# Optimization experiments

Hardware: AMD Instinct MI355X
Metric: run time of the kernel (lower is better)

## Reference

```python
import jax, jax.numpy as jnp
import numpy as np

DIM = 2048
NHEAD = 16
HEAD_DIM = DIM // NHEAD
FF_HIDDEN = 5632
EPS = 1e-6


def setup_inputs() -> dict:
    key = jax.random.key(0)
    ks = jax.random.split(key, 8)
    B, S = 2, 2048
    sd = 0.02
    return {
        "x": jax.random.normal(ks[0], (B, S, DIM), dtype=jnp.float32),
        "w_qkv": jax.random.normal(ks[1], (DIM, 3 * DIM), dtype=jnp.float32) * sd,
        "w_out": jax.random.normal(ks[2], (DIM, DIM), dtype=jnp.float32) * sd,
        "g1": jnp.ones((DIM,), dtype=jnp.float32),
        "g2": jnp.ones((DIM,), dtype=jnp.float32),
        "w1": jax.random.normal(ks[3], (DIM, FF_HIDDEN), dtype=jnp.float32) * sd,
        "w3": jax.random.normal(ks[4], (DIM, FF_HIDDEN), dtype=jnp.float32) * sd,
        "w2": jax.random.normal(ks[5], (FF_HIDDEN, DIM), dtype=jnp.float32) * sd,
    }


def _rmsnorm(x, g):
    rms = jnp.sqrt(jnp.mean(x * x, axis=-1, keepdims=True) + EPS)
    return x / rms * g


def _attention(x, w_qkv, w_out):
    B, S, D = x.shape
    qkv = x @ w_qkv  # [B,S,3D]
    q, k, v = jnp.split(qkv, 3, axis=-1)
    # [B,H,S,hd]
    q = q.reshape(B, S, NHEAD, HEAD_DIM).transpose(0, 2, 1, 3)
    k = k.reshape(B, S, NHEAD, HEAD_DIM).transpose(0, 2, 1, 3)
    v = v.reshape(B, S, NHEAD, HEAD_DIM).transpose(0, 2, 1, 3)
    scores = jnp.einsum("bhqd,bhkd->bhqk", q, k) / jnp.sqrt(jnp.float32(HEAD_DIM))
    causal = jnp.tril(jnp.ones((S, S), dtype=bool))
    scores = jnp.where(causal, scores, -jnp.inf)
    attn = jax.nn.softmax(scores, axis=-1)
    out = jnp.einsum("bhqk,bhkd->bhqd", attn, v)
    out = out.transpose(0, 2, 1, 3).reshape(B, S, D)
    return out @ w_out


def _swiglu(x, w1, w3, w2):
    return (jax.nn.silu(x @ w1) * (x @ w3)) @ w2


def reference(x, w_qkv, w_out, g1, g2, w1, w3, w2):
    x = x + _attention(_rmsnorm(x, g1), w_qkv, w_out)
    x = x + _swiglu(_rmsnorm(x, g2), w1, w3, w2)
    return x
```

## Files before the change

### kernel.cpp

```cpp
#include <hip/hip_runtime.h>
#include <hip/hip_bf16.h>
#include <stdint.h>


typedef __attribute__((ext_vector_type(8))) short bf16x8;
typedef __attribute__((ext_vector_type(8))) unsigned short u16x8;
typedef __attribute__((ext_vector_type(4))) float f32x4;

__device__ __forceinline__ unsigned short f2bf(float f) {
  union { float f; unsigned int u; } c; c.f = f;
  unsigned int u = c.u + 0x7fffu + ((c.u >> 16) & 1u);
  return (unsigned short)(u >> 16);
}
__device__ __forceinline__ float bf2f(unsigned short h) {
  union { unsigned int u; float f; } c; c.u = ((unsigned int)h) << 16;
  return c.f;
}

__device__ __forceinline__ void gload16(const void* g, void* l) {
  __builtin_amdgcn_global_load_lds(
      (const __attribute__((address_space(1))) void*)g,
      (__attribute__((address_space(3))) void*)l, 16, 0, 0);
}

__global__ __launch_bounds__(256)
void rmsnorm_bf16(const float* __restrict__ x, const float* __restrict__ g,
                  unsigned short* __restrict__ y)
{
  const long row = blockIdx.x;
  const float* xr = x + row * 2048;
  const int t = threadIdx.x;
  float4 a = *(const float4*)(xr + t * 8);
  float4 b = *(const float4*)(xr + t * 8 + 4);
  float ss = a.x*a.x + a.y*a.y + a.z*a.z + a.w*a.w
           + b.x*b.x + b.y*b.y + b.z*b.z + b.w*b.w;
#pragma unroll
  for (int off = 32; off >= 1; off >>= 1) ss += __shfl_xor(ss, off, 64);
  __shared__ float sm[4];
  if ((t & 63) == 0) sm[t >> 6] = ss;
  __syncthreads();
  float inv = rsqrtf((sm[0] + sm[1] + sm[2] + sm[3]) * (1.0f / 2048.0f) + 1e-6f);
  float4 ga = *(const float4*)(g + t * 8);
  float4 gb = *(const float4*)(g + t * 8 + 4);
  u16x8 ov;
  ov[0] = f2bf(a.x * inv * ga.x); ov[1] = f2bf(a.y * inv * ga.y);
  ov[2] = f2bf(a.z * inv * ga.z); ov[3] = f2bf(a.w * inv * ga.w);
  ov[4] = f2bf(b.x * inv * gb.x); ov[5] = f2bf(b.y * inv * gb.y);
  ov[6] = f2bf(b.z * inv * gb.z); ov[7] = f2bf(b.w * inv * gb.w);
  *(u16x8*)(y + row * 2048 + t * 8) = ov;
}

__global__ __launch_bounds__(256)
void transpose_w(const float* __restrict__ in, unsigned short* __restrict__ outp,
                 int K, int N)
{
  __shared__ float tile[32][33];
  const int c0 = blockIdx.x * 32, r0 = blockIdx.y * 32;
  const int cx = threadIdx.x & 31, ry = threadIdx.x >> 5;
#pragma unroll
  for (int i = 0; i < 4; i++)
    tile[ry + i * 8][cx] = in[(long)(r0 + ry + i * 8) * N + c0 + cx];
  __syncthreads();
#pragma unroll
  for (int i = 0; i < 4; i++)
    outp[(long)(c0 + ry + i * 8) * K + r0 + cx] = f2bf(tile[cx][ry + i * 8]);
}

__global__ __launch_bounds__(256)
void transpose_v(const unsigned short* __restrict__ qkv, unsigned short* __restrict__ vT)
{
  __shared__ unsigned short tile[32][34];
  const int bh = blockIdx.z, b = bh >> 4, hh = bh & 15;
  const int s0 = blockIdx.x * 32, d0 = blockIdx.y * 32;
  const int cx = threadIdx.x & 31, ry = threadIdx.x >> 5;
  const unsigned short* src = qkv + (long)b * 2048 * 6144 + 4096 + hh * 128;
#pragma unroll
  for (int i = 0; i < 4; i++)
    tile[ry + i * 8][cx] = src[(long)(s0 + ry + i * 8) * 6144 + d0 + cx];
  __syncthreads();
  unsigned short* o = vT + ((long)bh * 128 + d0) * 2048 + s0;
#pragma unroll
  for (int i = 0; i < 4; i++)
    o[(long)(ry + i * 8) * 2048 + cx] = tile[cx][ry + i * 8];
}

template<int EPI>
__global__ __launch_bounds__(256)
void gemm_bt(const unsigned short* __restrict__ A,
             const unsigned short* __restrict__ Bt,
             void* __restrict__ Cout,
             const float* __restrict__ res,
             const unsigned short* __restrict__ mulsrc,
             int M, int N, int K)
{
  __shared__ unsigned short lds[2 * 128 * 64];
  const int tid = threadIdx.x;
  const int lane = tid & 63, wave = tid >> 6;
  const int wr = wave >> 1, wc = wave & 1;
  const int l15 = lane & 15, lg = lane >> 4;

  const int nwg = gridDim.x * gridDim.y;
  int wg = blockIdx.y * gridDim.x + blockIdx.x;
  wg = (wg & 7) * (nwg >> 3) + (wg >> 3);
  const int bx = wg % gridDim.x, by = wg / gridDim.x;
  const long m0 = (long)by * 128, n0 = (long)bx * 128;

  f32x4 acc[4][4];
#pragma unroll
  for (int m = 0; m < 4; m++)
#pragma unroll
    for (int n = 0; n < 4; n++) acc[m][n] = f32x4{0.f, 0.f, 0.f, 0.f};

  const int rsub = lane >> 3;
  const int csw  = (lane & 7) ^ rsub;
  const unsigned short* Ab = A  + (m0 + wave * 32 + rsub) * (long)K + csw * 8;
  const unsigned short* Bb = Bt + (n0 + wave * 32 + rsub) * (long)K + csw * 8;
  unsigned short* Al = lds + wave * 2048;
  unsigned short* Bl = lds + 8192 + wave * 2048;

  for (int kt = 0; kt < K; kt += 64) {
    __syncthreads();
#pragma unroll
    for (int i = 0; i < 4; i++) {
      gload16(Ab + (long)(i * 8) * K + kt, Al + i * 512);
      gload16(Bb + (long)(i * 8) * K + kt, Bl + i * 512);
    }
    __syncthreads();
#pragma unroll
    for (int kc = 0; kc < 2; kc++) {
      bf16x8 af[4], bfr[4];
#pragma unroll
      for (int m = 0; m < 4; m++) {
        int row = wr * 64 + m * 16 + l15;
        int off = row * 128 + ((kc * 64 + lg * 16) ^ ((row & 7) << 4));
        af[m] = *(const bf16x8*)((const char*)lds + off);
      }
#pragma unroll
      for (int n = 0; n < 4; n++) {
        int row = wc * 64 + n * 16 + l15;
        int off = 16384 + row * 128 + ((kc * 64 + lg * 16) ^ ((row & 7) << 4));
        bfr[n] = *(const bf16x8*)((const char*)lds + off);
      }
#pragma unroll
      for (int m = 0; m < 4; m++)
#pragma unroll
        for (int n = 0; n < 4; n++)
          acc[m][n] = __builtin_amdgcn_mfma_f32_16x16x32_bf16(af[m], bfr[n], acc[m][n], 0, 0, 0);
    }
  }

  if (EPI == 3) {
#pragma unroll
    for (int m = 0; m < 4; m++)
#pragma unroll
      for (int n = 0; n < 4; n++)
#pragma unroll
        for (int r = 0; r < 4; r++) {
          long row = m0 + wr * 64 + m * 16 + lg * 4 + r;
          long col = n0 + wc * 64 + n * 16 + l15;
          ((float*)Cout)[row * N + col] = acc[m][n][r] + res[row * N + col];
        }
    return;
  }

  __syncthreads();
  unsigned short* Cl = lds;
#pragma unroll
  for (int m = 0; m < 4; m++)
#pragma unroll
    for (int n = 0; n < 4; n++)
#pragma unroll
      for (int r = 0; r < 4; r++) {
        float v = acc[m][n][r];
        if (EPI == 1) v = v / (1.f + __expf(-v));
        Cl[(wr * 64 + m * 16 + lg * 4 + r) * 128 + wc * 64 + n * 16 + l15] = f2bf(v);
      }
  __syncthreads();
#pragma unroll
  for (int r8 = 0; r8 < 8; r8++) {
    int id = tid + r8 * 256;
    int row = id >> 4, c = (id & 15) * 8;
    long grow = m0 + row, gcol = n0 + c;
    u16x8 v = *(const u16x8*)(Cl + row * 128 + c);
    if (EPI == 2) {
      u16x8 mm = *(const u16x8*)(mulsrc + grow * N + gcol);
#pragma unroll
      for (int j = 0; j < 8; j++) v[j] = f2bf(bf2f(v[j]) * bf2f(mm[j]));
    }
    *(u16x8*)((unsigned short*)Cout + grow * N + gcol) = v;
  }
}

#define QSTEP(qf, mrow, lrow, o, qb, isdiag) do {                              \
    f32x4 sacc[4];                                                             \
    __builtin_amdgcn_s_setprio(1);                                             \
    _Pragma("unroll")                                                          \
    for (int cg = 0; cg < 4; cg++) {                                           \
      f32x4 a = f32x4{0.f, 0.f, 0.f, 0.f};                                     \
      _Pragma("unroll")                                                        \
      for (int kc = 0; kc < 4; kc++) {                                         \
        int krow = cg * 16 + l15;                                              \
        bf16x8 kf = *(const bf16x8*)((char*)Klds +                             \
            (krow * 256 + ((kc * 64 + lg * 16) ^ ((krow & 7) << 4))));         \
        a = __builtin_amdgcn_mfma_f32_16x16x32_bf16(qf[kc], kf, a, 0, 0, 0);   \
      }                                                                        \
      sacc[cg] = a;                                                            \
    }                                                                          \
    __builtin_amdgcn_s_setprio(0);                                             \
    float p[4][4], pm[4];                                                      \
    _Pragma("unroll")                                                          \
    for (int r = 0; r < 4; r++) pm[r] = -1e30f;                                \
    _Pragma("unroll")                                                          \
    for (int cg = 0; cg < 4; cg++)                                             \
      _Pragma("unroll")                                                        \
      for (int r = 0; r < 4; r++) {                                            \
        float v = sacc[cg][r] * scale;                                         \
        if (isdiag) {                                                          \
          int kvg = kv0 + cg * 16 + l15;                                       \
          int qg = qb + w * 16 + lg * 4 + r;                                   \
          if (kvg > qg) v = -1e30f;                                            \
        }                                                                      \
        p[cg][r] = v;                                                          \
        pm[r] = fmaxf(pm[r], v);                                               \
      }                                                                        \
    _Pragma("unroll")                                                          \
    for (int r = 0; r < 4; r++) {                                              \
      _Pragma("unroll")                                                        \
      for (int off = 1; off < 16; off <<= 1)                                   \
        pm[r] = fmaxf(pm[r], __shfl_xor(pm[r], off, 64));                      \
      float mn = fmaxf(mrow[r], pm[r]);                                        \
      float al = __expf(mrow[r] - mn);                                         \
      mrow[r] = mn;                                                            \
      float s = 0.f;                                                           \
      _Pragma("unroll")                                                        \
      for (int cg = 0; cg < 4; cg++) { p[cg][r] = __expf(p[cg][r] - mn); s += p[cg][r]; } \
      _Pragma("unroll")                                                        \
      for (int off = 1; off < 16; off <<= 1)                                   \
        s += __shfl_xor(s, off, 64);                                           \
      lrow[r] = lrow[r] * al + s;                                              \
      _Pragma("unroll")                                                        \
      for (int dg = 0; dg < 8; dg++) o[dg][r] *= al;                           \
    }                                                                          \
    _Pragma("unroll")                                                          \
    for (int cg = 0; cg < 4; cg++)                                             \
      _Pragma("unroll")                                                        \
      for (int r = 0; r < 4; r++) {                                            \
        int q = lg * 4 + r;                                                    \
        *((unsigned short*)((char*)&Plds[w][0] +                               \
            (q * 128 + (((cg * 16 + l15) * 2) ^ ((q & 7) << 4))))) = f2bf(p[cg][r]); \
      }                                                                        \
    asm volatile("s_waitcnt lgkmcnt(0)" ::: "memory");                         \
    __builtin_amdgcn_sched_barrier(0);                                         \
    __builtin_amdgcn_s_setprio(1);                                             \
    _Pragma("unroll")                                                          \
    for (int kc = 0; kc < 2; kc++) {                                           \
      bf16x8 pa = *(const bf16x8*)((char*)&Plds[w][0] +                        \
          (l15 * 128 + ((kc * 64 + lg * 16) ^ ((l15 & 7) << 4))));             \
      _Pragma("unroll")                                                        \
      for (int dg = 0; dg < 8; dg++) {                                         \
        int d = dg * 16 + l15;                                                 \
        bf16x8 vf = *(const bf16x8*)((char*)Vlds +                             \
            (d * 128 + ((kc * 64 + lg * 16) ^ ((d & 7) << 4))));               \
        o[dg] = __builtin_amdgcn_mfma_f32_16x16x32_bf16(pa, vf, o[dg], 0, 0, 0); \
      }                                                                        \
    }                                                                          \
    __builtin_amdgcn_s_setprio(0);                                             \
  } while (0)

__global__ __launch_bounds__(256, 2)
void attn_fwd(const unsigned short* __restrict__ qkv,
              const unsigned short* __restrict__ vT,
              unsigned short* __restrict__ out)
{
  __shared__ unsigned short Klds[64 * 128];
  __shared__ unsigned short Vlds[128 * 64];
  __shared__ unsigned short Plds[4][16 * 64];
  const int tid = threadIdx.x, lane = tid & 63, w = tid >> 6;
  const int l15 = lane & 15, lg = lane >> 4;

  const int nwg = gridDim.x * gridDim.y;
  int wg = blockIdx.y * gridDim.x + blockIdx.x;
  wg = (wg & 7) * (nwg >> 3) + (wg >> 3);
  const int ip = wg % 16;
  const int bh = wg / 16;
  const int b = bh >> 4, hh = bh & 15;

  const int qbA = ip * 64, qbB = (31 - ip) * 64;
  const long base = (long)b * 2048 * 6144;
  const int qoff = hh * 128, koff = 2048 + hh * 128;
  const unsigned short* vTg = vT + (long)bh * (128 * 2048);

  bf16x8 qfA[4], qfB[4];
  {
    long qrA = qbA + w * 16 + l15, qrB = qbB + w * 16 + l15;
#pragma unroll
    for (int kc = 0; kc < 4; kc++) {
      qfA[kc] = *(const bf16x8*)(qkv + base + qrA * 6144 + qoff + kc * 32 + lg * 8);
      qfB[kc] = *(const bf16x8*)(qkv + base + qrB * 6144 + qoff + kc * 32 + lg * 8);
    }
  }
  f32x4 oA[8], oB[8];
#pragma unroll
  for (int dg = 0; dg < 8; dg++) {
    oA[dg] = f32x4{0.f, 0.f, 0.f, 0.f};
    oB[dg] = f32x4{0.f, 0.f, 0.f, 0.f};
  }
  float mA[4] = {-1e30f, -1e30f, -1e30f, -1e30f}, lA[4] = {0.f, 0.f, 0.f, 0.f};
  float mB[4] = {-1e30f, -1e30f, -1e30f, -1e30f}, lB[4] = {0.f, 0.f, 0.f, 0.f};
  const float scale = 0.08838834764831845f;

  const int s_st = tid >> 4, d0 = (tid & 15) * 8;
  const int vrow = tid >> 3, vc = tid & 7;

  const int nt = 32 - ip;
  for (int t = 0; t < nt; t++) {
    const int kv0 = t * 64;
#pragma unroll
    for (int u = 0; u < 4; u++) {
      int srow = s_st + u * 16;
      uint4 kk = *(const uint4*)(qkv + base + (long)(kv0 + srow) * 6144 + koff + d0);
      *(uint4*)((char*)Klds + (srow * 256 + ((d0 * 2) ^ ((srow & 7) << 4)))) = kk;
    }
#pragma unroll
    for (int u = 0; u < 4; u++) {
      int d = vrow + u * 32;
      uint4 vv = *(const uint4*)(vTg + (long)d * 2048 + kv0 + vc * 8);
      *(uint4*)((char*)Vlds + (d * 128 + ((vc * 16) ^ ((d & 7) << 4)))) = vv;
    }
    __syncthreads();

    if (t <= ip) QSTEP(qfA, mA, lA, oA, qbA, (t == ip));
    QSTEP(qfB, mB, lB, oB, qbB, (t == nt - 1));

    __syncthreads();
  }

#pragma unroll
  for (int r = 0; r < 4; r++) {
    float invA = 1.f / lA[r], invB = 1.f / lB[r];
    long rowA = (long)b * 2048 + qbA + w * 16 + lg * 4 + r;
    long rowB = (long)b * 2048 + qbB + w * 16 + lg * 4 + r;
#pragma unroll
    for (int dg = 0; dg < 8; dg++) {
      out[rowA * 2048 + hh * 128 + dg * 16 + l15] = f2bf(oA[dg][r] * invA);
      out[rowB * 2048 + hh * 128 + dg * 16 + l15] = f2bf(oB[dg][r] * invB);
    }
  }
}

extern "C" void kernel_launch(void* const* d_in, const int* in_sizes, int n_in,
                              void* d_out, int out_size, void* d_ws, size_t ws_size,
                              hipStream_t stream)
{
  const float* x     = (const float*)d_in[0];
  const float* w_qkv = (const float*)d_in[1];
  const float* w_out = (const float*)d_in[2];
  const float* g1    = (const float*)d_in[3];
  const float* g2    = (const float*)d_in[4];
  const float* w1    = (const float*)d_in[5];
  const float* w3    = (const float*)d_in[6];
  const float* w2    = (const float*)d_in[7];
  float* outp = (float*)d_out;
  char* ws = (char*)d_ws;

  unsigned short* wT  = (unsigned short*)(ws);
  unsigned short* y   = (unsigned short*)(ws + 25165824);
  unsigned short* qkv = (unsigned short*)(ws + 41943040);
  unsigned short* att = (unsigned short*)(ws + 92274688);
  float*          x1  = (float*)(ws + 109051904);
  unsigned short* s1  = (unsigned short*)(ws + 142606336);
  unsigned short* vTb = s1;
  unsigned short* h   = qkv;

  rmsnorm_bf16<<<4096, 256, 0, stream>>>(x, g1, y);
  transpose_w<<<dim3(6144 / 32, 2048 / 32), 256, 0, stream>>>(w_qkv, wT, 2048, 6144);
  gemm_bt<0><<<dim3(48, 32), 256, 0, stream>>>(y, wT, qkv, nullptr, nullptr, 4096, 6144, 2048);
  transpose_v<<<dim3(64, 4, 32), 256, 0, stream>>>(qkv, vTb);
  attn_fwd<<<dim3(16, 32), 256, 0, stream>>>(qkv, vTb, att);
  transpose_w<<<dim3(64, 64), 256, 0, stream>>>(w_out, wT, 2048, 2048);
  gemm_bt<3><<<dim3(16, 32), 256, 0, stream>>>(att, wT, x1, x, nullptr, 4096, 2048, 2048);

  rmsnorm_bf16<<<4096, 256, 0, stream>>>(x1, g2, y);
  transpose_w<<<dim3(176, 64), 256, 0, stream>>>(w1, wT, 2048, 5632);
  gemm_bt<1><<<dim3(44, 32), 256, 0, stream>>>(y, wT, s1, nullptr, nullptr, 4096, 5632, 2048);
  transpose_w<<<dim3(176, 64), 256, 0, stream>>>(w3, wT, 2048, 5632);
  gemm_bt<2><<<dim3(44, 32), 256, 0, stream>>>(y, wT, h, nullptr, s1, 4096, 5632, 2048);
  transpose_w<<<dim3(64, 176), 256, 0, stream>>>(w2, wT, 5632, 2048);
  gemm_bt<3><<<dim3(16, 32), 256, 0, stream>>>(h, wT, outp, x1, nullptr, 4096, 2048, 5632);
}
```

Measured before the change: 716.5 us.

## Add 256x256-tile 8-wave pipelined GEMM for QKV and FFN up projections

Adds a new GEMM kernel that uses 256x256 output tiles with 512 threads, a double-buffered 128KB LDS, swizzled layout, explicit vmcnt/barrier scheduling and raised MFMA priority. It replaces the 128x128 kernel for the QKV, w1 and w3 projections. The aim is more data reuse per LDS load and overlap of global loads with MFMA work. The cost is fewer workgroups (a 384 or 352 block grid), which may leave CUs idle at the tail, plus heavy register and LDS pressure per block.

```diff
diff --git a/kernel.cpp b/kernel.cpp
--- a/kernel.cpp
+++ b/kernel.cpp
@@ -84,6 +84,177 @@
     o[(long)(ry + i * 8) * 2048 + cx] = tile[cx][ry + i * 8];
 }
 
+#define PH_BAR __builtin_amdgcn_s_barrier()
+#define LGKM0 asm volatile("s_waitcnt lgkmcnt(0)" ::: "memory")
+#define VM6 asm volatile("s_waitcnt vmcnt(6)" ::: "memory")
+#define VM0 asm volatile("s_waitcnt vmcnt(0)" ::: "memory")
+
+#define REG_A(buf, kk) ((buf) * 65536 + (kk) * 16384)
+#define REG_B(buf, kk) (32768 + (buf) * 65536 + (kk) * 16384)
+
+#define LDA4(buf, kk, mg) { \
+  a[0] = *(const bf16x8*)(L + REG_A(buf, kk) + aoff + ((mg) + 0) * 1024); \
+  a[1] = *(const bf16x8*)(L + REG_A(buf, kk) + aoff + ((mg) + 1) * 1024); \
+  a[2] = *(const bf16x8*)(L + REG_A(buf, kk) + aoff + ((mg) + 2) * 1024); \
+  a[3] = *(const bf16x8*)(L + REG_A(buf, kk) + aoff + ((mg) + 3) * 1024); }
+
+#define LDB4(buf, kk) { \
+  b[0] = *(const bf16x8*)(L + REG_B(buf, kk) + boff + 0 * 1024); \
+  b[1] = *(const bf16x8*)(L + REG_B(buf, kk) + boff + 1 * 1024); \
+  b[2] = *(const bf16x8*)(L + REG_B(buf, kk) + boff + 2 * 1024); \
+  b[3] = *(const bf16x8*)(L + REG_B(buf, kk) + boff + 3 * 1024); }
+
+#define MM16(mg) { \
+  __builtin_amdgcn_s_setprio(1); \
+  _Pragma("unroll") for (int j = 0; j < 4; j++) \
+    _Pragma("unroll") for (int n = 0; n < 4; n++) \
+      acc[(mg) + j][n] = __builtin_amdgcn_mfma_f32_16x16x32_bf16(a[j], b[n], acc[(mg) + j][n], 0, 0, 0); \
+  __builtin_amdgcn_s_setprio(0); }
+
+#define STGA(buf, kk, tt) { \
+  gload16(As + (long)(tt) * 64 + (kk) * 32,         L + REG_A(buf, kk) + sdst); \
+  gload16(As + rstep + (long)(tt) * 64 + (kk) * 32, L + REG_A(buf, kk) + 8192 + sdst); }
+#define STGB(buf, kk, tt) { \
+  gload16(Bs + (long)(tt) * 64 + (kk) * 32,         L + REG_B(buf, kk) + sdst); \
+  gload16(Bs + rstep + (long)(tt) * 64 + (kk) * 32, L + REG_B(buf, kk) + 8192 + sdst); }
+
+template<int EPI>
+__global__ __launch_bounds__(512, 2)
+void gemm256(const unsigned short* __restrict__ A,
+             const unsigned short* __restrict__ Bt,
+             void* __restrict__ Cout,
+             const float* __restrict__ res,
+             const unsigned short* __restrict__ mulsrc,
+             int M, int N, int K)
+{
+  __shared__ alignas(16) char L[131072];
+  const int tid = threadIdx.x;
+  const int lane = tid & 63, wave = tid >> 6;
+  const int wr = wave >> 2, wc = wave & 3;
+  const int l15 = lane & 15, lg = lane >> 4;
+
+  const int nwg = gridDim.x * gridDim.y;
+  int wg = blockIdx.y * gridDim.x + blockIdx.x;
+  wg = (wg & 7) * (nwg >> 3) + (wg >> 3);
+  const int bx = wg % gridDim.x, by = wg / gridDim.x;
+  const long m0 = (long)by * 256, n0 = (long)bx * 256;
+
+  f32x4 acc[8][4];
+#pragma unroll
+  for (int m = 0; m < 8; m++)
+#pragma unroll
+    for (int n = 0; n < 4; n++) acc[m][n] = f32x4{0.f, 0.f, 0.f, 0.f};
+
+  const int row0 = tid >> 2, cc = tid & 3;
+  const int csw = cc ^ ((row0 >> 1) & 3);
+  const unsigned short* As = A + (m0 + row0) * (long)K + csw * 8;
+  const unsigned short* Bs = Bt + (n0 + row0) * (long)K + csw * 8;
+  const long rstep = (long)128 * K;
+  const int sdst = wave * 1024;
+
+  const int swz = (lg ^ ((l15 >> 1) & 3)) << 4;
+  const int aoff = wr * 8192 + l15 * 64 + swz;
+  const int boff = wc * 4096 + l15 * 64 + swz;
+
+  const int nkt = K >> 6, nit = nkt >> 1;
+
+  STGB(0, 0, 0); STGA(0, 0, 0); STGB(0, 1, 0); STGA(0, 1, 0);
+  STGB(1, 0, 1); STGA(1, 0, 1); STGB(1, 1, 1);
+  VM6;
+  PH_BAR;
+  __builtin_amdgcn_sched_barrier(0);
+
+  for (int it = 0; it < nit; ++it) {
+    const int T = 2 * it;
+    const bool full = (it < nit - 1);
+    bf16x8 a[4], b[4];
+    LDB4(0, 0) LDA4(0, 0, 0)
+    STGA(1, 1, T + 1)
+    PH_BAR; LGKM0;
+    MM16(0)
+    PH_BAR;
+    LDA4(0, 0, 4)
+    if (full) STGB(0, 0, T + 2)
+    PH_BAR; LGKM0;
+    MM16(4)
+    PH_BAR;
+    LDB4(0, 1) LDA4(0, 1, 0)
+    if (full) STGA(0, 0, T + 2)
+    PH_BAR; LGKM0;
+    MM16(0)
+    PH_BAR;
+    LDA4(0, 1, 4)
+    if (full) STGB(0, 1, T + 2)
+    PH_BAR; LGKM0;
+    MM16(4)
+    if (full) { VM6; } else { VM0; }
+    PH_BAR;
+    __builtin_amdgcn_sched_barrier(0);
+    LDB4(1, 0) LDA4(1, 0, 0)
+    if (full) STGA(0, 1, T + 2)
+    PH_BAR; LGKM0;
+    MM16(0)
+    PH_BAR;
+    LDA4(1, 0, 4)
+    if (full) STGB(1, 0, T + 3)
+    PH_BAR; LGKM0;
+    MM16(4)
+    PH_BAR;
+    LDB4(1, 1) LDA4(1, 1, 0)
+    if (full) STGA(1, 0, T + 3)
+    PH_BAR; LGKM0;
+    MM16(0)
+    PH_BAR;
+    LDA4(1, 1, 4)
+    if (full) STGB(1, 1, T + 3)
+    PH_BAR; LGKM0;
+    MM16(4)
+    if (full) { VM6; }
+    PH_BAR;
+    __builtin_amdgcn_sched_barrier(0);
+  }
+
+  if (EPI == 3) {
+#pragma unroll
+    for (int m = 0; m < 8; m++)
+#pragma unroll
+      for (int n = 0; n < 4; n++)
+#pragma unroll
+        for (int r = 0; r < 4; r++) {
+          long row = m0 + wr * 128 + m * 16 + lg * 4 + r;
+          long col = n0 + wc * 64 + n * 16 + l15;
+          ((float*)Cout)[row * N + col] = acc[m][n][r] + res[row * N + col];
+        }
+    return;
+  }
+
+#pragma unroll
+  for (int m = 0; m < 8; m++)
+#pragma unroll
+    for (int n = 0; n < 4; n++)
+#pragma unroll
+      for (int r = 0; r < 4; r++) {
+        float v = acc[m][n][r];
+        if (EPI == 1) v = v / (1.f + __expf(-v));
+        *(unsigned short*)(L + (wr * 128 + m * 16 + lg * 4 + r) * 512
+                             + (wc * 64 + n * 16 + l15) * 2) = f2bf(v);
+      }
+  __syncthreads();
+#pragma unroll
+  for (int rnd = 0; rnd < 16; rnd++) {
+    int id = tid + rnd * 512;
+    int row = id >> 5, c = (id & 31) * 8;
+    u16x8 v = *(const u16x8*)(L + row * 512 + c * 2);
+    long grow = m0 + row, gcol = n0 + c;
+    if (EPI == 2) {
+      u16x8 mm = *(const u16x8*)(mulsrc + grow * N + gcol);
+#pragma unroll
+      for (int j = 0; j < 8; j++) v[j] = f2bf(bf2f(v[j]) * bf2f(mm[j]));
+    }
+    *(u16x8*)((unsigned short*)Cout + grow * N + gcol) = v;
+  }
+}
+
 template<int EPI>
 __global__ __launch_bounds__(256)
 void gemm_bt(const unsigned short* __restrict__ A,
@@ -112,8 +283,8 @@
     for (int n = 0; n < 4; n++) acc[m][n] = f32x4{0.f, 0.f, 0.f, 0.f};
 
   const int rsub = lane >> 3;
-  const int csw  = (lane & 7) ^ rsub;
-  const unsigned short* Ab = A  + (m0 + wave * 32 + rsub) * (long)K + csw * 8;
+  const int csw = (lane & 7) ^ rsub;
+  const unsigned short* Ab = A + (m0 + wave * 32 + rsub) * (long)K + csw * 8;
   const unsigned short* Bb = Bt + (n0 + wave * 32 + rsub) * (long)K + csw * 8;
   unsigned short* Al = lds + wave * 2048;
   unsigned short* Bl = lds + 8192 + wave * 2048;
@@ -373,8 +544,8 @@
   unsigned short* h   = qkv;
 
   rmsnorm_bf16<<<4096, 256, 0, stream>>>(x, g1, y);
-  transpose_w<<<dim3(6144 / 32, 2048 / 32), 256, 0, stream>>>(w_qkv, wT, 2048, 6144);
-  gemm_bt<0><<<dim3(48, 32), 256, 0, stream>>>(y, wT, qkv, nullptr, nullptr, 4096, 6144, 2048);
+  transpose_w<<<dim3(192, 64), 256, 0, stream>>>(w_qkv, wT, 2048, 6144);
+  gemm256<0><<<dim3(24, 16), 512, 0, stream>>>(y, wT, qkv, nullptr, nullptr, 4096, 6144, 2048);
   transpose_v<<<dim3(64, 4, 32), 256, 0, stream>>>(qkv, vTb);
   attn_fwd<<<dim3(16, 32), 256, 0, stream>>>(qkv, vTb, att);
   transpose_w<<<dim3(64, 64), 256, 0, stream>>>(w_out, wT, 2048, 2048);
@@ -382,9 +553,9 @@
 
   rmsnorm_bf16<<<4096, 256, 0, stream>>>(x1, g2, y);
   transpose_w<<<dim3(176, 64), 256, 0, stream>>>(w1, wT, 2048, 5632);
-  gemm_bt<1><<<dim3(44, 32), 256, 0, stream>>>(y, wT, s1, nullptr, nullptr, 4096, 5632, 2048);
+  gemm256<1><<<dim3(22, 16), 512, 0, stream>>>(y, wT, s1, nullptr, nullptr, 4096, 5632, 2048);
   transpose_w<<<dim3(176, 64), 256, 0, stream>>>(w3, wT, 2048, 5632);
-  gemm_bt<2><<<dim3(44, 32), 256, 0, stream>>>(y, wT, h, nullptr, s1, 4096, 5632, 2048);
+  gemm256<2><<<dim3(22, 16), 512, 0, stream>>>(y, wT, h, nullptr, s1, 4096, 5632, 2048);
   transpose_w<<<dim3(64, 176), 256, 0, stream>>>(w2, wT, 5632, 2048);
   gemm_bt<3><<<dim3(16, 32), 256, 0, stream>>>(h, wT, outp, x1, nullptr, 4096, 2048, 5632);
 }
```

Measured after the change: 715.4 us. No clear change (-0.2%).

## Fuse W1/W3 GEMMs into one SwiGLU kernel and double-buffer attention K/V

Applied to the files above, without the earlier changes.

Replaces the two separate FFN up-projection GEMMs, which round-tripped the silu output through memory, with one kernel. It loads the activation tile once and accumulates both W1 and W3 products, then applies silu*mul in the epilogue. Attention now double-buffers K/V tiles in LDS, prefetching the next tile into registers during compute and dropping one barrier per iteration. The trade-off is more registers and LDS per block (two accumulator sets, 48KB LDS), which may lower occupancy.

```diff
diff --git a/kernel.cpp b/kernel.cpp
--- a/kernel.cpp
+++ b/kernel.cpp
@@ -90,7 +90,6 @@
              const unsigned short* __restrict__ Bt,
              void* __restrict__ Cout,
              const float* __restrict__ res,
-             const unsigned short* __restrict__ mulsrc,
              int M, int N, int K)
 {
   __shared__ unsigned short lds[2 * 128 * 64];
@@ -112,8 +111,8 @@
     for (int n = 0; n < 4; n++) acc[m][n] = f32x4{0.f, 0.f, 0.f, 0.f};
 
   const int rsub = lane >> 3;
-  const int csw  = (lane & 7) ^ rsub;
-  const unsigned short* Ab = A  + (m0 + wave * 32 + rsub) * (long)K + csw * 8;
+  const int csw = (lane & 7) ^ rsub;
+  const unsigned short* Ab = A + (m0 + wave * 32 + rsub) * (long)K + csw * 8;
   const unsigned short* Bb = Bt + (n0 + wave * 32 + rsub) * (long)K + csw * 8;
   unsigned short* Al = lds + wave * 2048;
   unsigned short* Bl = lds + 8192 + wave * 2048;
@@ -170,11 +169,8 @@
 #pragma unroll
     for (int n = 0; n < 4; n++)
 #pragma unroll
-      for (int r = 0; r < 4; r++) {
-        float v = acc[m][n][r];
-        if (EPI == 1) v = v / (1.f + __expf(-v));
-        Cl[(wr * 64 + m * 16 + lg * 4 + r) * 128 + wc * 64 + n * 16 + l15] = f2bf(v);
-      }
+      for (int r = 0; r < 4; r++)
+        Cl[(wr * 64 + m * 16 + lg * 4 + r) * 128 + wc * 64 + n * 16 + l15] = f2bf(acc[m][n][r]);
   __syncthreads();
 #pragma unroll
   for (int r8 = 0; r8 < 8; r8++) {
@@ -182,16 +178,109 @@
     int row = id >> 4, c = (id & 15) * 8;
     long grow = m0 + row, gcol = n0 + c;
     u16x8 v = *(const u16x8*)(Cl + row * 128 + c);
-    if (EPI == 2) {
-      u16x8 mm = *(const u16x8*)(mulsrc + grow * N + gcol);
-#pragma unroll
-      for (int j = 0; j < 8; j++) v[j] = f2bf(bf2f(v[j]) * bf2f(mm[j]));
-    }
     *(u16x8*)((unsigned short*)Cout + grow * N + gcol) = v;
   }
 }
 
-#define QSTEP(qf, mrow, lrow, o, qb, isdiag) do {                              \
+__global__ __launch_bounds__(256)
+void gemm_w13(const unsigned short* __restrict__ A,
+              const unsigned short* __restrict__ B1t,
+              const unsigned short* __restrict__ B3t,
+              unsigned short* __restrict__ H,
+              int M, int N, int K)
+{
+  __shared__ unsigned short lds[3 * 128 * 64];
+  const int tid = threadIdx.x;
+  const int lane = tid & 63, wave = tid >> 6;
+  const int wr = wave >> 1, wc = wave & 1;
+  const int l15 = lane & 15, lg = lane >> 4;
+
+  const int nwg = gridDim.x * gridDim.y;
+  int wg = blockIdx.y * gridDim.x + blockIdx.x;
+  wg = (wg & 7) * (nwg >> 3) + (wg >> 3);
+  const int bx = wg % gridDim.x, by = wg / gridDim.x;
+  const long m0 = (long)by * 128, n0 = (long)bx * 128;
+
+  f32x4 acc1[4][4], acc3[4][4];
+#pragma unroll
+  for (int m = 0; m < 4; m++)
+#pragma unroll
+    for (int n = 0; n < 4; n++) {
+      acc1[m][n] = f32x4{0.f, 0.f, 0.f, 0.f};
+      acc3[m][n] = f32x4{0.f, 0.f, 0.f, 0.f};
+    }
+
+  const int rsub = lane >> 3;
+  const int csw = (lane & 7) ^ rsub;
+  const unsigned short* Ab  = A   + (m0 + wave * 32 + rsub) * (long)K + csw * 8;
+  const unsigned short* B1b = B1t + (n0 + wave * 32 + rsub) * (long)K + csw * 8;
+  const unsigned short* B3b = B3t + (n0 + wave * 32 + rsub) * (long)K + csw * 8;
+  unsigned short* Al  = lds + wave * 2048;
+  unsigned short* B1l = lds + 8192 + wave * 2048;
+  unsigned short* B3l = lds + 16384 + wave * 2048;
+
+  for (int kt = 0; kt < K; kt += 64) {
+    __syncthreads();
+#pragma unroll
+    for (int i = 0; i < 4; i++) {
+      gload16(Ab  + (long)(i * 8) * K + kt, Al  + i * 512);
+      gload16(B1b + (long)(i * 8) * K + kt, B1l + i * 512);
+      gload16(B3b + (long)(i * 8) * K + kt, B3l + i * 512);
+    }
+    __syncthreads();
+#pragma unroll
+    for (int kc = 0; kc < 2; kc++) {
+      bf16x8 af[4], b1[4], b3[4];
+#pragma unroll
+      for (int m = 0; m < 4; m++) {
+        int row = wr * 64 + m * 16 + l15;
+        int off = row * 128 + ((kc * 64 + lg * 16) ^ ((row & 7) << 4));
+        af[m] = *(const bf16x8*)((const char*)lds + off);
+      }
+#pragma unroll
+      for (int n = 0; n < 4; n++) {
+        int row = wc * 64 + n * 16 + l15;
+        int off = row * 128 + ((kc * 64 + lg * 16) ^ ((row & 7) << 4));
+        b1[n] = *(const bf16x8*)((const char*)lds + 16384 + off);
+        b3[n] = *(const bf16x8*)((const char*)lds + 32768 + off);
+      }
+#pragma unroll
+      for (int m = 0; m < 4; m++) {
+#pragma unroll
+        for (int n = 0; n < 4; n++)
+          acc1[m][n] = __builtin_amdgcn_mfma_f32_16x16x32_bf16(af[m], b1[n], acc1[m][n], 0, 0, 0);
+#pragma unroll
+        for (int n = 0; n < 4; n++)
+          acc3[m][n] = __builtin_amdgcn_mfma_f32_16x16x32_bf16(af[m], b3[n], acc3[m][n], 0, 0, 0);
+      }
+    }
+  }
+
+  __syncthreads();
+  unsigned short* Cl = lds;
+#pragma unroll
+  for (int m = 0; m < 4; m++)
+#pragma unroll
+    for (int n = 0; n < 4; n++)
+#pragma unroll
+      for (int r = 0; r < 4; r++) {
+        float v1 = acc1[m][n][r];
+        float s = v1 / (1.f + __expf(-v1));
+        Cl[(wr * 64 + m * 16 + lg * 4 + r) * 128 + wc * 64 + n * 16 + l15] =
+            f2bf(s * acc3[m][n][r]);
+      }
+  __syncthreads();
+#pragma unroll
+  for (int r8 = 0; r8 < 8; r8++) {
+    int id = tid + r8 * 256;
+    int row = id >> 4, c = (id & 15) * 8;
+    long grow = m0 + row, gcol = n0 + c;
+    u16x8 v = *(const u16x8*)(Cl + row * 128 + c);
+    *(u16x8*)(H + grow * N + gcol) = v;
+  }
+}
+
+#define QSTEP(qf, mrow, lrow, o, qb, isdiag, Kb, Vb) do {                      \
     f32x4 sacc[4];                                                             \
     __builtin_amdgcn_s_setprio(1);                                             \
     _Pragma("unroll")                                                          \
@@ -200,7 +289,7 @@
       _Pragma("unroll")                                                        \
       for (int kc = 0; kc < 4; kc++) {                                         \
         int krow = cg * 16 + l15;                                              \
-        bf16x8 kf = *(const bf16x8*)((char*)Klds +                             \
+        bf16x8 kf = *(const bf16x8*)((const char*)(Kb) +                       \
             (krow * 256 + ((kc * 64 + lg * 16) ^ ((krow & 7) << 4))));         \
         a = __builtin_amdgcn_mfma_f32_16x16x32_bf16(qf[kc], kf, a, 0, 0, 0);   \
       }                                                                        \
@@ -259,7 +348,7 @@
       _Pragma("unroll")                                                        \
       for (int dg = 0; dg < 8; dg++) {                                         \
         int d = dg * 16 + l15;                                                 \
-        bf16x8 vf = *(const bf16x8*)((char*)Vlds +                             \
+        bf16x8 vf = *(const bf16x8*)((const char*)(Vb) +                       \
             (d * 128 + ((kc * 64 + lg * 16) ^ ((d & 7) << 4))));               \
         o[dg] = __builtin_amdgcn_mfma_f32_16x16x32_bf16(pa, vf, o[dg], 0, 0, 0); \
       }                                                                        \
@@ -272,8 +361,8 @@
               const unsigned short* __restrict__ vT,
               unsigned short* __restrict__ out)
 {
-  __shared__ unsigned short Klds[64 * 128];
-  __shared__ unsigned short Vlds[128 * 64];
+  __shared__ unsigned short K2[2][64 * 128];
+  __shared__ unsigned short V2[2][128 * 64];
   __shared__ unsigned short Plds[4][16 * 64];
   const int tid = threadIdx.x, lane = tid & 63, w = tid >> 6;
   const int l15 = lane & 15, lg = lane >> 4;
@@ -313,26 +402,53 @@
   const int vrow = tid >> 3, vc = tid & 7;
 
   const int nt = 32 - ip;
+  uint4 kr[4], vr[4];
+
+#pragma unroll
+  for (int u = 0; u < 4; u++) {
+    kr[u] = *(const uint4*)(qkv + base + (long)(s_st + u * 16) * 6144 + koff + d0);
+    vr[u] = *(const uint4*)(vTg + (long)(vrow + u * 32) * 2048 + vc * 8);
+  }
+#pragma unroll
+  for (int u = 0; u < 4; u++) {
+    int srow = s_st + u * 16;
+    *(uint4*)((char*)&K2[0][0] + (srow * 256 + ((d0 * 2) ^ ((srow & 7) << 4)))) = kr[u];
+    int d = vrow + u * 32;
+    *(uint4*)((char*)&V2[0][0] + (d * 128 + ((vc * 16) ^ ((d & 7) << 4)))) = vr[u];
+  }
+  __syncthreads();
+
+  int cur = 0;
   for (int t = 0; t < nt; t++) {
     const int kv0 = t * 64;
-#pragma unroll
-    for (int u = 0; u < 4; u++) {
-      int srow = s_st + u * 16;
-      uint4 kk = *(const uint4*)(qkv + base + (long)(kv0 + srow) * 6144 + koff + d0);
-      *(uint4*)((char*)Klds + (srow * 256 + ((d0 * 2) ^ ((srow & 7) << 4)))) = kk;
-    }
-#pragma unroll
-    for (int u = 0; u < 4; u++) {
-      int d = vrow + u * 32;
-      uint4 vv = *(const uint4*)(vTg + (long)d * 2048 + kv0 + vc * 8);
-      *(uint4*)((char*)Vlds + (d * 128 + ((vc * 16) ^ ((d & 7) << 4)))) = vv;
+    const bool more = (t + 1 < nt);
+    if (more) {
+      const long kvb = base + (long)((t + 1) * 64) * 6144;
+#pragma unroll
+      for (int u = 0; u < 4; u++) {
+        kr[u] = *(const uint4*)(qkv + kvb + (long)(s_st + u * 16) * 6144 + koff + d0);
+        vr[u] = *(const uint4*)(vTg + (long)(vrow + u * 32) * 2048 + (t + 1) * 64 + vc * 8);
+      }
+    }
+
+    const char* Kb = (const char*)&K2[cur][0];
+    const char* Vb = (const char*)&V2[cur][0];
+    if (t <= ip) QSTEP(qfA, mA, lA, oA, qbA, (t == ip), Kb, Vb);
+    QSTEP(qfB, mB, lB, oB, qbB, (t == nt - 1), Kb, Vb);
+
+    if (more) {
+      char* Kn = (char*)&K2[cur ^ 1][0];
+      char* Vn = (char*)&V2[cur ^ 1][0];
+#pragma unroll
+      for (int u = 0; u < 4; u++) {
+        int srow = s_st + u * 16;
+        *(uint4*)(Kn + (srow * 256 + ((d0 * 2) ^ ((srow & 7) << 4)))) = kr[u];
+        int d = vrow + u * 32;
+        *(uint4*)(Vn + (d * 128 + ((vc * 16) ^ ((d & 7) << 4)))) = vr[u];
+      }
     }
     __syncthreads();
-
-    if (t <= ip) QSTEP(qfA, mA, lA, oA, qbA, (t == ip));
-    QSTEP(qfB, mB, lB, oB, qbB, (t == nt - 1));
-
-    __syncthreads();
+    cur ^= 1;
   }
 
 #pragma unroll
@@ -368,23 +484,22 @@
   unsigned short* qkv = (unsigned short*)(ws + 41943040);
   unsigned short* att = (unsigned short*)(ws + 92274688);
   float*          x1  = (float*)(ws + 109051904);
-  unsigned short* s1  = (unsigned short*)(ws + 142606336);
-  unsigned short* vTb = s1;
+  unsigned short* wT2 = (unsigned short*)(ws + 142606336);
+  unsigned short* vTb = wT2;
   unsigned short* h   = qkv;
 
   rmsnorm_bf16<<<4096, 256, 0, stream>>>(x, g1, y);
-  transpose_w<<<dim3(6144 / 32, 2048 / 32), 256, 0, stream>>>(w_qkv, wT, 2048, 6144);
-  gemm_bt<0><<<dim3(48, 32), 256, 0, stream>>>(y, wT, qkv, nullptr, nullptr, 4096, 6144, 2048);
+  transpose_w<<<dim3(192, 64), 256, 0, stream>>>(w_qkv, wT, 2048, 6144);
+  gemm_bt<0><<<dim3(48, 32), 256, 0, stream>>>(y, wT, qkv, nullptr, 4096, 6144, 2048);
   transpose_v<<<dim3(64, 4, 32), 256, 0, stream>>>(qkv, vTb);
   attn_fwd<<<dim3(16, 32), 256, 0, stream>>>(qkv, vTb, att);
   transpose_w<<<dim3(64, 64), 256, 0, stream>>>(w_out, wT, 2048, 2048);
-  gemm_bt<3><<<dim3(16, 32), 256, 0, stream>>>(att, wT, x1, x, nullptr, 4096, 2048, 2048);
+  gemm_bt<3><<<dim3(16, 32), 256, 0, stream>>>(att, wT, x1, x, 4096, 2048, 2048);
 
   rmsnorm_bf16<<<4096, 256, 0, stream>>>(x1, g2, y);
   transpose_w<<<dim3(176, 64), 256, 0, stream>>>(w1, wT, 2048, 5632);
-  gemm_bt<1><<<dim3(44, 32), 256, 0, stream>>>(y, wT, s1, nullptr, nullptr, 4096, 5632, 2048);
-  transpose_w<<<dim3(176, 64), 256, 0, stream>>>(w3, wT, 2048, 5632);
-  gemm_bt<2><<<dim3(44, 32), 256, 0, stream>>>(y, wT, h, nullptr, s1, 4096, 5632, 2048);
+  transpose_w<<<dim3(176, 64), 256, 0, stream>>>(w3, wT2, 2048, 5632);
+  gemm_w13<<<dim3(44, 32), 256, 0, stream>>>(y, wT, wT2, h, 4096, 5632, 2048);
   transpose_w<<<dim3(64, 176), 256, 0, stream>>>(w2, wT, 5632, 2048);
-  gemm_bt<3><<<dim3(16, 32), 256, 0, stream>>>(h, wT, outp, x1, nullptr, 4096, 2048, 5632);
-}
+  gemm_bt<3><<<dim3(16, 32), 256, 0, stream>>>(h, wT, outp, x1, 4096, 2048, 5632);
+}
```

Result: slower. 889.0 us (+24.1%).
